# Kernel optimization log

Measured on AMD Instinct MI355X. Metric: run time of the kernel, lower is better.

The kernel has to match this reference:

```python
import jax, jax.numpy as jnp
import numpy as np

N_NODES = 65536
N_EDGES = 524288
N_LAYERS = 3
D = 128
ED = 32
BATCH = 64
NEG_SLOPE = 0.2


def setup_inputs() -> dict:
    key = jax.random.key(0)
    ks = jax.random.split(key, 10)
    w_scale = 1.0 / np.sqrt(D)
    return {
        "x": jax.random.normal(ks[0], (N_NODES, D), dtype=jnp.float32),
        "edge_index": jax.random.randint(ks[1], (2, N_EDGES), 0, N_NODES, dtype=jnp.int32),
        "edge_attr": jax.random.normal(ks[2], (N_EDGES, ED), dtype=jnp.float32),
        "Ws": jax.random.normal(ks[3], (N_LAYERS, D, D), dtype=jnp.float32) * w_scale,
        "att_src": jax.random.normal(ks[4], (N_LAYERS, D), dtype=jnp.float32) * w_scale,
        "att_dst": jax.random.normal(ks[5], (N_LAYERS, D), dtype=jnp.float32) * w_scale,
        "W_edge": jax.random.normal(ks[6], (N_LAYERS, ED, D), dtype=jnp.float32) * (1.0 / np.sqrt(ED)),
        "att_edge": jax.random.normal(ks[7], (N_LAYERS, D), dtype=jnp.float32) * w_scale,
        "bias": jnp.zeros((N_LAYERS, D), dtype=jnp.float32),
        "batch_size": BATCH,
    }


def _gat_layer(x, src, dst, ea, W, a_s, a_d, We, a_e, b, n):
    # PyG GATConv, heads=1, concat=True, flow source_to_target.
    h = x @ W                                      # [N, D]
    al = (h @ a_s)[src] + (h @ a_d)[dst] + (ea @ We) @ a_e   # [E]
    al = jax.nn.leaky_relu(al, NEG_SLOPE)
    # segment softmax over destination-node neighborhoods
    m = jax.ops.segment_max(al, dst, num_segments=n)
    ex = jnp.exp(al - m[dst])
    den = jax.ops.segment_sum(ex, dst, num_segments=n)
    w = ex / den[dst]                              # [E]
    out = jax.ops.segment_sum(w[:, None] * h[src], dst, num_segments=n)
    return out + b


def reference(x, edge_index, edge_attr, Ws, att_src, att_dst, W_edge, att_edge, bias, batch_size):
    n = x.shape[0]
    # add_self_loops with fill_value='mean': self-loop edge_attr is the mean of
    # incoming edge features per destination node (zero if no incoming edges).
    loop = jnp.arange(n, dtype=edge_index.dtype)
    src = jnp.concatenate([edge_index[0], loop])
    dst = jnp.concatenate([edge_index[1], loop])
    cnt = jax.ops.segment_sum(jnp.ones((edge_attr.shape[0],), edge_attr.dtype), edge_index[1], num_segments=n)
    fill = jax.ops.segment_sum(edge_attr, edge_index[1], num_segments=n) / jnp.maximum(cnt, 1.0)[:, None]
    ea = jnp.concatenate([edge_attr, fill], axis=0)

    h = x
    for l in range(Ws.shape[0]):
        h = jax.nn.gelu(
            _gat_layer(h, src, dst, ea, Ws[l], att_src[l], att_dst[l], W_edge[l], att_edge[l], bias[l], n),
            approximate=False,
        )
        # dropout p=0.2 is identity in eval mode
    return h.reshape(batch_size, n // batch_size, -1)
```

## Files before the change

### kernel.cpp

```cpp
#include <hip/hip_runtime.h>
#include <math.h>

#define NN 65536
#define NE 524288
#define D 128
#define ED 32
#define NEG_SLOPE 0.2f

typedef short bf16x8 __attribute__((ext_vector_type(8)));
typedef float f32x4 __attribute__((ext_vector_type(4)));
typedef unsigned short ushort_t;

__device__ __forceinline__ float leaky(float x) { return x > 0.f ? x : NEG_SLOPE * x; }
__device__ __forceinline__ float gelu_exact(float x) {
    return 0.5f * x * (1.f + erff(x * 0.70710678118654752440f));
}
__device__ __forceinline__ unsigned short bf16_rne(float x) {
    unsigned u = __float_as_uint(x);
    return (unsigned short)((u + 0x7FFFu + ((u >> 16) & 1u)) >> 16);
}
__device__ __forceinline__ void unpack8(int4 r, float* f) {
    unsigned u0 = (unsigned)r.x, u1 = (unsigned)r.y, u2 = (unsigned)r.z, u3 = (unsigned)r.w;
    f[0] = __uint_as_float(u0 << 16); f[1] = __uint_as_float(u0 & 0xFFFF0000u);
    f[2] = __uint_as_float(u1 << 16); f[3] = __uint_as_float(u1 & 0xFFFF0000u);
    f[4] = __uint_as_float(u2 << 16); f[5] = __uint_as_float(u2 & 0xFFFF0000u);
    f[6] = __uint_as_float(u3 << 16); f[7] = __uint_as_float(u3 & 0xFFFF0000u);
}


__global__ __launch_bounds__(256) void k_front(const float* __restrict__ ea,
        const int* __restrict__ srcArr,
        const float* __restrict__ We, const float* __restrict__ ae,
        const float* __restrict__ Ws, short* __restrict__ Whp, short* __restrict__ Wlp,
        int4* __restrict__ edata_eo) {
    if (blockIdx.x >= NE / 256) {
        int t = (blockIdx.x - NE / 256) * 256 + threadIdx.x;
        if (t >= 3 * 4 * 4 * 128) return;
        int n = t & 127;
        int q = (t >> 7) & 3;
        int ks = (t >> 9) & 3;
        int l = t >> 11;
        const float* w = Ws + (size_t)l * D * D;
        size_t obase = (size_t)l * D * D + ((size_t)((ks * 4 + q) * 128) + n) * 8;
        #pragma unroll
        for (int j = 0; j < 8; ++j) {
            float x = w[(size_t)(ks * 32 + q * 8 + j) * D + n];
            unsigned short hb = bf16_rne(x);
            float hf = __uint_as_float(((unsigned)hb) << 16);
            Whp[obase + j] = (short)hb;
            Wlp[obase + j] = (short)bf16_rne(x - hf);
        }
        return;
    }
    __shared__ __align__(16) float wv[3 * ED];
    int t = threadIdx.x;
    if (t < 3 * ED) {
        int l = t >> 5, k = t & 31;
        const float4* w = (const float4*)(We + (size_t)(l * ED + k) * D);
        const float4* a = (const float4*)(ae + (size_t)l * D);
        float s = 0.f;
        #pragma unroll
        for (int i = 0; i < D / 4; ++i) {
            float4 x = w[i], y = a[i];
            s += x.x * y.x + x.y * y.y + x.z * y.z + x.w * y.w;
        }
        wv[t] = s;
    }
    __syncthreads();

    int c = (t & 7) * 4;
    float4 wl0 = *(const float4*)(wv + c);
    float4 wl1 = *(const float4*)(wv + ED + c);
    float4 wl2 = *(const float4*)(wv + 2 * ED + c);
    const float4* eab = (const float4*)(ea + (size_t)blockIdx.x * 256 * ED);
    int rbase = blockIdx.x * 256;
    #pragma unroll
    for (int i = 0; i < 8; ++i) {
        float4 v = eab[i * 256 + t];
        float p0 = v.x * wl0.x + v.y * wl0.y + v.z * wl0.z + v.w * wl0.w;
        float p1 = v.x * wl1.x + v.y * wl1.y + v.z * wl1.z + v.w * wl1.w;
        float p2 = v.x * wl2.x + v.y * wl2.y + v.z * wl2.z + v.w * wl2.w;
        #pragma unroll
        for (int off = 1; off < 8; off <<= 1) {
            p0 += __shfl_xor(p0, off);
            p1 += __shfl_xor(p1, off);
            p2 += __shfl_xor(p2, off);
        }
        if ((t & 7) == 0) {
            int r = rbase + i * 32 + (t >> 3);
            edata_eo[r] = make_int4(srcArr[r], __float_as_int(p0),
                                    __float_as_int(p1), __float_as_int(p2));
        }
    }
}


__device__ __forceinline__ void gemm_body(int b, const float* __restrict__ A,
        const short* __restrict__ Whp, const short* __restrict__ Wlp,
        const float* __restrict__ a_s, const float* __restrict__ a_d,
        ushort_t* __restrict__ Hb, float* __restrict__ als, float* __restrict__ ald) {
    __shared__ int4 Bs[2048];
    int t = threadIdx.x;
    int wave = t >> 6, lane = t & 63;
    int l16 = lane & 15, q = lane >> 4;
    int rows_base = b * 64 + wave * 16;

    const int4* wh4 = (const int4*)Whp;
    const int4* wl4 = (const int4*)Wlp;
    const short* bsh = (const short*)Bs;
    const short* bsl = (const short*)(Bs + 1024);

    f32x4 acc[8] = {};
    #pragma unroll
    for (int h2 = 0; h2 < 2; ++h2) {
        if (h2) __syncthreads();
        #pragma unroll
        for (int i = 0; i < 4; ++i) {
            Bs[t + 256 * i] = wh4[h2 * 1024 + t + 256 * i];
            Bs[1024 + t + 256 * i] = wl4[h2 * 1024 + t + 256 * i];
        }
        __syncthreads();
        #pragma unroll
        for (int kk = 0; kk < 2; ++kk) {
            int ks = h2 * 2 + kk;
            const float* ap = A + (size_t)(rows_base + l16) * D + ks * 32 + q * 8;
            float4 v0 = *(const float4*)ap;
            float4 v1 = *(const float4*)(ap + 4);
            float f[8] = {v0.x, v0.y, v0.z, v0.w, v1.x, v1.y, v1.z, v1.w};
            bf16x8 ah, alo;
            #pragma unroll
            for (int j = 0; j < 8; ++j) {
                unsigned short hb = bf16_rne(f[j]);
                float hf = __uint_as_float(((unsigned)hb) << 16);
                ah[j]  = (short)hb;
                alo[j] = (short)bf16_rne(f[j] - hf);
            }
            #pragma unroll
            for (int nt = 0; nt < 8; ++nt) {
                int idx = (((kk * 4 + q) * 128) + nt * 16 + l16) * 8;
                bf16x8 bh = *(const bf16x8*)(bsh + idx);
                bf16x8 bl = *(const bf16x8*)(bsl + idx);
                acc[nt] = __builtin_amdgcn_mfma_f32_16x16x32_bf16(bh, ah, acc[nt], 0, 0, 0);
                acc[nt] = __builtin_amdgcn_mfma_f32_16x16x32_bf16(bl, ah, acc[nt], 0, 0, 0);
                acc[nt] = __builtin_amdgcn_mfma_f32_16x16x32_bf16(bh, alo, acc[nt], 0, 0, 0);
            }
        }
    }

    float ps = 0.f, pd = 0.f;
    #pragma unroll
    for (int nt = 0; nt < 8; ++nt) {
        float4 a4 = *(const float4*)(a_s + nt * 16 + q * 4);
        float4 d4 = *(const float4*)(a_d + nt * 16 + q * 4);
        ps += acc[nt][0] * a4.x + acc[nt][1] * a4.y + acc[nt][2] * a4.z + acc[nt][3] * a4.w;
        pd += acc[nt][0] * d4.x + acc[nt][1] * d4.y + acc[nt][2] * d4.z + acc[nt][3] * d4.w;
    }
    ps += __shfl_xor(ps, 16); pd += __shfl_xor(pd, 16);
    ps += __shfl_xor(ps, 32); pd += __shfl_xor(pd, 32);
    if (q == 0) {
        als[rows_base + l16] = ps;
        ald[rows_base + l16] = pd;
    }

    __syncthreads();
    char* tb = (char*)Bs + wave * 4096;
    {
        int row = l16;
        unsigned key = (unsigned)(row & 7) << 4;
        #pragma unroll
        for (int nt = 0; nt < 8; ++nt) {
            ushort4 pk;
            pk.x = bf16_rne(acc[nt][0]);
            pk.y = bf16_rne(acc[nt][1]);
            pk.z = bf16_rne(acc[nt][2]);
            pk.w = bf16_rne(acc[nt][3]);
            unsigned byteoff = (unsigned)row * 256u + (unsigned)(nt * 16 + q * 4) * 2u;
            *(ushort4*)(tb + (byteoff ^ key)) = pk;
        }
    }
    __syncthreads();
    #pragma unroll
    for (int i = 0; i < 4; ++i) {
        int m = lane + 64 * i;
        unsigned row = (unsigned)m >> 4;
        unsigned byteoff = (unsigned)m * 16u;
        unsigned addr = byteoff ^ ((row & 7u) << 4);
        int4 v = *(const int4*)(tb + addr);
        *(int4*)((char*)Hb + (size_t)rows_base * 256 + (size_t)m * 16) = v;
    }
}


__global__ __launch_bounds__(256) void k_h1g0(const int* __restrict__ dstArr,
        int* __restrict__ C,
        const float* __restrict__ x, const short* __restrict__ Whp,
        const short* __restrict__ Wlp, const float* __restrict__ a_s,
        const float* __restrict__ a_d, ushort_t* __restrict__ Hb,
        float* __restrict__ als, float* __restrict__ ald) {
    int t = threadIdx.x;
    if (blockIdx.x < 512) {
        __shared__ int hist[256];
        hist[t] = 0;
        __syncthreads();
        int base = blockIdx.x * 1024;
        #pragma unroll
        for (int i = 0; i < 4; ++i) {
            int d = dstArr[base + i * 256 + t];
            atomicAdd(&hist[d >> 8], 1);
        }
        __syncthreads();
        C[blockIdx.x * 256 + t] = hist[t];
        return;
    }
    gemm_body(blockIdx.x - 512, x, Whp, Wlp, a_s, a_d, Hb, als, ald);
}


__global__ __launch_bounds__(256) void k_scanA(int* __restrict__ C, int* __restrict__ T) {
    __shared__ int s[512];
    int t = threadIdx.x, h = blockIdx.x;
    int a0 = C[t * 256 + h];
    int a1 = C[(t + 256) * 256 + h];
    s[t] = a0; s[t + 256] = a1;
    __syncthreads();
    for (int off = 1; off < 512; off <<= 1) {
        int v0 = (t >= off) ? s[t - off] : 0;
        int v1 = (t + 256 >= off) ? s[t + 256 - off] : 0;
        __syncthreads();
        s[t] += v0; s[t + 256] += v1;
        __syncthreads();
    }
    C[t * 256 + h] = s[t] - a0;
    C[(t + 256) * 256 + h] = s[t + 256] - a1;
    if (t == 255) T[h] = s[511];
}


__global__ __launch_bounds__(256) void k_scanB(const int* __restrict__ T, int* __restrict__ H,
                                               int* __restrict__ rp) {
    __shared__ int s[256];
    int t = threadIdx.x;
    int v = T[t];
    s[t] = v;
    __syncthreads();
    for (int off = 1; off < 256; off <<= 1) {
        int x = (t >= off) ? s[t - off] : 0;
        __syncthreads();
        s[t] += x;
        __syncthreads();
    }
    H[t] = s[t] - v;
    if (t == 255) { H[256] = s[255]; rp[NN] = s[255]; }
}


__global__ __launch_bounds__(256) void k_rank1(const int* __restrict__ dstArr,
        const int4* __restrict__ edata_eo, const int* __restrict__ C,
        const int* __restrict__ H, int4* __restrict__ eordR, int* __restrict__ eordD) {
    __shared__ int base[256];
    __shared__ int cnt[256];
    int t = threadIdx.x, b = blockIdx.x;
    base[t] = C[b * 256 + t] + H[t];
    cnt[t] = 0;
    __syncthreads();
    #pragma unroll
    for (int i = 0; i < 4; ++i) {
        int e = b * 1024 + i * 256 + t;
        int d = dstArr[e];
        int4 rec = edata_eo[e];
        int hi = d >> 8;
        int r = atomicAdd(&cnt[hi], 1);
        int p = base[hi] + r;
        eordR[p] = rec;
        eordD[p] = d;
    }
}


__global__ __launch_bounds__(256) void k_rank2(const int* __restrict__ eordD,
        const int4* __restrict__ eordR, const int* __restrict__ H,
        int4* __restrict__ edata, int* __restrict__ rp) {
    __shared__ int h2[256];
    __shared__ int sc[256];
    __shared__ int cnt[256];
    int t = threadIdx.x, h = blockIdx.x;
    int s0 = H[h], s1 = H[h + 1];
    h2[t] = 0; cnt[t] = 0;
    __syncthreads();
    for (int i = s0 + t; i < s1; i += 256) atomicAdd(&h2[eordD[i] & 255], 1);
    __syncthreads();
    int v = h2[t];
    sc[t] = v;
    __syncthreads();
    for (int off = 1; off < 256; off <<= 1) {
        int x = (t >= off) ? sc[t - off] : 0;
        __syncthreads();
        sc[t] += x;
        __syncthreads();
    }
    int baseLo = sc[t] - v;
    rp[h * 256 + t] = s0 + baseLo;
    __syncthreads();
    sc[t] = baseLo;
    __syncthreads();
    for (int i = s0 + t; i < s1; i += 256) {
        int d = eordD[i];
        int4 rec = eordR[i];
        int lo = d & 255;
        int r = atomicAdd(&cnt[lo], 1);
        edata[s0 + sc[lo] + r] = rec;
    }
}


__global__ __launch_bounds__(256) void k_gemm(const float* __restrict__ A,
        const short* __restrict__ Whp, const short* __restrict__ Wlp,
        const float* __restrict__ a_s, const float* __restrict__ a_d,
        ushort_t* __restrict__ Hb, float* __restrict__ als, float* __restrict__ ald) {
    gemm_body(blockIdx.x, A, Whp, Wlp, a_s, a_d, Hb, als, ald);
}


__global__ __launch_bounds__(256) void k_aggr(const ushort_t* __restrict__ hb,
        const float* __restrict__ als, const float* __restrict__ ald,
        const int4* __restrict__ edata, const int* __restrict__ rp,
        const float* __restrict__ bias, int lsel, float* __restrict__ out_f32) {
    int t = threadIdx.x;
    int lane = t & 63;
    int l16 = lane & 15;
    int qb = lane & 48;
    int n = blockIdx.x * 16 + (t >> 4);
    int s = rp[n], e = rp[n + 1];
    int deg = e - s;
    float aldd = ald[n];
    float alsn = als[n];
    float inv_deg = (deg > 0) ? 1.f / (float)deg : 0.f;

    int4 hvp = *(const int4*)(hb + (size_t)n * D + l16 * 8);
    float acc8[8];

    if (deg <= 16) {
        int sn0 = 0;
        float alev0 = 0.f, alsg = 0.f;
        if (l16 < deg) {
            int4 ed = edata[s + l16];
            sn0 = ed.x;
            alev0 = __int_as_float((lsel == 0) ? ed.y : ((lsel == 1) ? ed.z : ed.w));
            alsg = als[sn0];
        }

        int sA[8], sB[8];
        #pragma unroll
        for (int i = 0; i < 8; ++i) { sA[i] = __shfl(sn0, qb + i); sB[i] = __shfl(sn0, qb + 8 + i); }
        int4 rb[8];
        #pragma unroll
        for (int i = 0; i < 8; ++i) rb[i] = *(const int4*)(hb + (size_t)sA[i] * D + l16 * 8);
        bool more = (deg > 8);
        int4 rb2[8];
        if (more) {
            #pragma unroll
            for (int i = 0; i < 8; ++i) rb2[i] = *(const int4*)(hb + (size_t)sB[i] * D + l16 * 8);
        }

        float al0 = (l16 < deg) ? leaky(alsg + aldd + alev0) : -1e30f;
        float mm = al0, asum = alev0;
        #pragma unroll
        for (int off = 1; off < 16; off <<= 1) {
            mm = fmaxf(mm, __shfl_xor(mm, off));
            asum += __shfl_xor(asum, off);
        }
        float self_al = leaky(alsn + aldd + asum * inv_deg);
        mm = fmaxf(mm, self_al);
        float p0 = (l16 < deg) ? __expf(al0 - mm) : 0.f;
        float den = p0;
        #pragma unroll
        for (int off = 1; off < 16; off <<= 1) den += __shfl_xor(den, off);
        float es = __expf(self_al - mm);
        den += es;
        float inv = 1.f / den;
        float w0 = p0 * inv;
        float wself = es * inv;

        float fv[8];
        unpack8(hvp, fv);
        #pragma unroll
        for (int j = 0; j < 8; ++j) acc8[j] = wself * fv[j];

        float wA[8], wB[8];
        #pragma unroll
        for (int i = 0; i < 8; ++i) { wA[i] = __shfl(w0, qb + i); wB[i] = __shfl(w0, qb + 8 + i); }

        #pragma unroll
        for (int i = 0; i < 8; ++i) {
            float f[8];
            unpack8(rb[i], f);
            #pragma unroll
            for (int j = 0; j < 8; ++j) acc8[j] += wA[i] * f[j];
        }
        if (more) {
            #pragma unroll
            for (int i = 0; i < 8; ++i) {
                float f[8];
                unpack8(rb2[i], f);
                #pragma unroll
                for (int j = 0; j < 8; ++j) acc8[j] += wB[i] * f[j];
            }
        }
    } else {
        float mm = -1e30f, asum = 0.f;
        for (int base = s; base < e; base += 16) {
            int j = base + l16;
            if (j < e) {
                int4 ed = edata[j];
                float alev = __int_as_float((lsel == 0) ? ed.y : ((lsel == 1) ? ed.z : ed.w));
                asum += alev;
                mm = fmaxf(mm, leaky(als[ed.x] + aldd + alev));
            }
        }
        #pragma unroll
        for (int off = 1; off < 16; off <<= 1) {
            mm = fmaxf(mm, __shfl_xor(mm, off));
            asum += __shfl_xor(asum, off);
        }
        float self_al = leaky(alsn + aldd + asum * inv_deg);
        mm = fmaxf(mm, self_al);
        float den = 0.f;
        for (int base = s; base < e; base += 16) {
            int j = base + l16;
            if (j < e) {
                int4 ed = edata[j];
                float alev = __int_as_float((lsel == 0) ? ed.y : ((lsel == 1) ? ed.z : ed.w));
                den += __expf(leaky(als[ed.x] + aldd + alev) - mm);
            }
        }
        #pragma unroll
        for (int off = 1; off < 16; off <<= 1) den += __shfl_xor(den, off);
        float es = __expf(self_al - mm);
        den += es;
        float inv = 1.f / den;
        float wself = es * inv;
        float fv[8];
        unpack8(hvp, fv);
        #pragma unroll
        for (int j = 0; j < 8; ++j) acc8[j] = wself * fv[j];
        for (int base = s; base < e; base += 16) {
            int cnt = min(e - base, 16);
            int sn = 0;
            float w = 0.f;
            if (l16 < cnt) {
                int4 ed = edata[base + l16];
                sn = ed.x;
                float alev = __int_as_float((lsel == 0) ? ed.y : ((lsel == 1) ? ed.z : ed.w));
                w = __expf(leaky(als[sn] + aldd + alev) - mm) * inv;
            }
            for (int tt = 0; tt < cnt; ++tt) {
                int st = __shfl(sn, qb + tt);
                float wt = __shfl(w, qb + tt);
                int4 r = *(const int4*)(hb + (size_t)st * D + l16 * 8);
                float f[8];
                unpack8(r, f);
                #pragma unroll
                for (int j = 0; j < 8; ++j) acc8[j] += wt * f[j];
            }
        }
    }

    const float4* b4 = (const float4*)(bias + l16 * 8);
    float4 b0 = b4[0], b1 = b4[1];
    float bb[8] = {b0.x, b0.y, b0.z, b0.w, b1.x, b1.y, b1.z, b1.w};
    float o[8];
    #pragma unroll
    for (int j = 0; j < 8; ++j) o[j] = gelu_exact(acc8[j] + bb[j]);

    float4* o4 = (float4*)(out_f32 + (size_t)n * D + l16 * 8);
    o4[0] = make_float4(o[0], o[1], o[2], o[3]);
    o4[1] = make_float4(o[4], o[5], o[6], o[7]);
}


extern "C" void kernel_launch(void* const* d_in, const int* in_sizes, int n_in,
                              void* d_out, int out_size, void* d_ws, size_t ws_size,
                              hipStream_t stream) {
    (void)in_sizes; (void)n_in; (void)out_size; (void)ws_size;
    const float* x        = (const float*)d_in[0];
    const int*   eidx     = (const int*)d_in[1];
    const float* ea       = (const float*)d_in[2];
    const float* Ws       = (const float*)d_in[3];
    const float* att_src  = (const float*)d_in[4];
    const float* att_dst  = (const float*)d_in[5];
    const float* W_edge   = (const float*)d_in[6];
    const float* att_edge = (const float*)d_in[7];
    const float* bias     = (const float*)d_in[8];
    float* out = (float*)d_out;

    char* ws = (char*)d_ws;
    size_t off = 0;
    auto alloc = [&](size_t bytes) {
        void* p = ws + off;
        off += (bytes + 255) & ~(size_t)255;
        return p;
    };
    ushort_t* Hb   = (ushort_t*)alloc((size_t)NN * D * 2);
    float*    Hx   = (float*)alloc((size_t)NN * D * 4);
    float*    als  = (float*)alloc((size_t)NN * 4);
    float*    ald  = (float*)alloc((size_t)NN * 4);
    int4*     edata= (int4*)alloc((size_t)(NE + 16) * 16);
    int4*     edata_eo = (int4*)alloc((size_t)NE * 16);
    int4*     eordR = (int4*)alloc((size_t)NE * 16);
    int*      eordD = (int*)alloc((size_t)NE * 4);
    int*      C    = (int*)alloc((size_t)512 * 256 * 4);
    int*      T    = (int*)alloc(256 * 4);
    int*      H    = (int*)alloc(260 * 4);
    int*      rp   = (int*)alloc((size_t)(NN + 4) * 4);
    short*    Whp  = (short*)alloc((size_t)3 * D * D * 2);
    short*    Wlp  = (short*)alloc((size_t)3 * D * D * 2);

    const int* e_src = eidx;
    const int* e_dst = eidx + NE;

    k_front<<<NE / 256 + 24, 256, 0, stream>>>(ea, e_src, W_edge, att_edge,
                                               Ws, Whp, Wlp, edata_eo);
    k_h1g0<<<512 + NN / 64, 256, 0, stream>>>(e_dst, C, x, Whp, Wlp, att_src, att_dst,
                                              Hb, als, ald);
    k_scanA<<<256, 256, 0, stream>>>(C, T);
    k_scanB<<<256 / 256, 256, 0, stream>>>(T, H, rp);
    k_rank1<<<512, 256, 0, stream>>>(e_dst, edata_eo, C, H, eordR, eordD);
    k_rank2<<<256, 256, 0, stream>>>(eordD, eordR, H, edata, rp);

    for (int l = 0; l < 3; ++l) {
        bool last = (l == 2);
        k_aggr<<<NN / 16, 256, 0, stream>>>(Hb, als, ald, edata, rp, bias + (size_t)l * D, l,
                                            last ? out : Hx);
        if (!last) {
            k_gemm<<<NN / 64, 256, 0, stream>>>(Hx, Whp + (size_t)(l + 1) * D * D,
                                                Wlp + (size_t)(l + 1) * D * D,
                                                att_src + (size_t)(l + 1) * D,
                                                att_dst + (size_t)(l + 1) * D,
                                                Hb, als, ald);
        }
    }
}
```

Before: 349.9 us.

## Fuse edge-attention projection into partition scatter and drop intermediate edge buffer

The edge-attribute projection onto the three per-layer edge attention vectors now happens inside the bucket-scatter kernel. Each block computes the projections and writes the packed records straight into their destination-bucketed slots, so the separate edge-record buffer no longer has to be written and read back. The destination histogram and weight packing move into a small first kernel that runs before the scans. The scatter is fused with the first-layer GEMM in a single launch so the two can overlap. In exchange, each scatter block walks 1024 edges serially with only one lane in eight doing atomics, and the order of edges within a bucket changes.

```diff
diff --git a/kernel.cpp b/kernel.cpp
--- a/kernel.cpp
+++ b/kernel.cpp
@@ -28,70 +28,78 @@
 }
 
 
-__global__ __launch_bounds__(256) void k_front(const float* __restrict__ ea,
-        const int* __restrict__ srcArr,
-        const float* __restrict__ We, const float* __restrict__ ae,
-        const float* __restrict__ Ws, short* __restrict__ Whp, short* __restrict__ Wlp,
-        int4* __restrict__ edata_eo) {
-    if (blockIdx.x >= NE / 256) {
-        int t = (blockIdx.x - NE / 256) * 256 + threadIdx.x;
-        if (t >= 3 * 4 * 4 * 128) return;
-        int n = t & 127;
-        int q = (t >> 7) & 3;
-        int ks = (t >> 9) & 3;
-        int l = t >> 11;
-        const float* w = Ws + (size_t)l * D * D;
-        size_t obase = (size_t)l * D * D + ((size_t)((ks * 4 + q) * 128) + n) * 8;
-        #pragma unroll
-        for (int j = 0; j < 8; ++j) {
-            float x = w[(size_t)(ks * 32 + q * 8 + j) * D + n];
-            unsigned short hb = bf16_rne(x);
-            float hf = __uint_as_float(((unsigned)hb) << 16);
-            Whp[obase + j] = (short)hb;
-            Wlp[obase + j] = (short)bf16_rne(x - hf);
-        }
+__global__ __launch_bounds__(256) void k_hist_wpack(const int* __restrict__ dstArr,
+        int* __restrict__ C, const float* __restrict__ Ws,
+        short* __restrict__ Whp, short* __restrict__ Wlp) {
+    int t = threadIdx.x;
+    if (blockIdx.x < 512) {
+        __shared__ int hist[256];
+        hist[t] = 0;
+        __syncthreads();
+        int base = blockIdx.x * 1024;
+        #pragma unroll
+        for (int i = 0; i < 4; ++i) {
+            int d = dstArr[base + i * 256 + t];
+            atomicAdd(&hist[d >> 8], 1);
+        }
+        __syncthreads();
+        C[blockIdx.x * 256 + t] = hist[t];
         return;
     }
-    __shared__ __align__(16) float wv[3 * ED];
+    int tt = (blockIdx.x - 512) * 256 + t;
+    if (tt >= 3 * 4 * 4 * 128) return;
+    int n = tt & 127;
+    int q = (tt >> 7) & 3;
+    int ks = (tt >> 9) & 3;
+    int l = tt >> 11;
+    const float* w = Ws + (size_t)l * D * D;
+    size_t obase = (size_t)l * D * D + ((size_t)((ks * 4 + q) * 128) + n) * 8;
+    #pragma unroll
+    for (int j = 0; j < 8; ++j) {
+        float x = w[(size_t)(ks * 32 + q * 8 + j) * D + n];
+        unsigned short hb = bf16_rne(x);
+        float hf = __uint_as_float(((unsigned)hb) << 16);
+        Whp[obase + j] = (short)hb;
+        Wlp[obase + j] = (short)bf16_rne(x - hf);
+    }
+}
+
+
+__global__ __launch_bounds__(256) void k_scanA(int* __restrict__ C, int* __restrict__ T) {
+    __shared__ int s[512];
+    int t = threadIdx.x, h = blockIdx.x;
+    int a0 = C[t * 256 + h];
+    int a1 = C[(t + 256) * 256 + h];
+    s[t] = a0; s[t + 256] = a1;
+    __syncthreads();
+    for (int off = 1; off < 512; off <<= 1) {
+        int v0 = (t >= off) ? s[t - off] : 0;
+        int v1 = (t + 256 >= off) ? s[t + 256 - off] : 0;
+        __syncthreads();
+        s[t] += v0; s[t + 256] += v1;
+        __syncthreads();
+    }
+    C[t * 256 + h] = s[t] - a0;
+    C[(t + 256) * 256 + h] = s[t + 256] - a1;
+    if (t == 255) T[h] = s[511];
+}
+
+
+__global__ __launch_bounds__(256) void k_scanB(const int* __restrict__ T, int* __restrict__ H,
+                                               int* __restrict__ rp) {
+    __shared__ int s[256];
     int t = threadIdx.x;
-    if (t < 3 * ED) {
-        int l = t >> 5, k = t & 31;
-        const float4* w = (const float4*)(We + (size_t)(l * ED + k) * D);
-        const float4* a = (const float4*)(ae + (size_t)l * D);
-        float s = 0.f;
-        #pragma unroll
-        for (int i = 0; i < D / 4; ++i) {
-            float4 x = w[i], y = a[i];
-            s += x.x * y.x + x.y * y.y + x.z * y.z + x.w * y.w;
-        }
-        wv[t] = s;
-    }
-    __syncthreads();
-
-    int c = (t & 7) * 4;
-    float4 wl0 = *(const float4*)(wv + c);
-    float4 wl1 = *(const float4*)(wv + ED + c);
-    float4 wl2 = *(const float4*)(wv + 2 * ED + c);
-    const float4* eab = (const float4*)(ea + (size_t)blockIdx.x * 256 * ED);
-    int rbase = blockIdx.x * 256;
-    #pragma unroll
-    for (int i = 0; i < 8; ++i) {
-        float4 v = eab[i * 256 + t];
-        float p0 = v.x * wl0.x + v.y * wl0.y + v.z * wl0.z + v.w * wl0.w;
-        float p1 = v.x * wl1.x + v.y * wl1.y + v.z * wl1.z + v.w * wl1.w;
-        float p2 = v.x * wl2.x + v.y * wl2.y + v.z * wl2.z + v.w * wl2.w;
-        #pragma unroll
-        for (int off = 1; off < 8; off <<= 1) {
-            p0 += __shfl_xor(p0, off);
-            p1 += __shfl_xor(p1, off);
-            p2 += __shfl_xor(p2, off);
-        }
-        if ((t & 7) == 0) {
-            int r = rbase + i * 32 + (t >> 3);
-            edata_eo[r] = make_int4(srcArr[r], __float_as_int(p0),
-                                    __float_as_int(p1), __float_as_int(p2));
-        }
-    }
+    int v = T[t];
+    s[t] = v;
+    __syncthreads();
+    for (int off = 1; off < 256; off <<= 1) {
+        int x = (t >= off) ? s[t - off] : 0;
+        __syncthreads();
+        s[t] += x;
+        __syncthreads();
+    }
+    H[t] = s[t] - v;
+    if (t == 255) { H[256] = s[255]; rp[NN] = s[255]; }
 }
 
 
@@ -191,89 +199,68 @@
 }
 
 
-__global__ __launch_bounds__(256) void k_h1g0(const int* __restrict__ dstArr,
-        int* __restrict__ C,
+__global__ __launch_bounds__(256) void k_partgemm(const float* __restrict__ ea,
+        const int* __restrict__ srcArr, const int* __restrict__ dstArr,
+        const float* __restrict__ We, const float* __restrict__ ae,
+        const int* __restrict__ C, const int* __restrict__ H,
+        int4* __restrict__ eordR, int* __restrict__ eordD,
         const float* __restrict__ x, const short* __restrict__ Whp,
         const short* __restrict__ Wlp, const float* __restrict__ a_s,
         const float* __restrict__ a_d, ushort_t* __restrict__ Hb,
         float* __restrict__ als, float* __restrict__ ald) {
     int t = threadIdx.x;
     if (blockIdx.x < 512) {
-        __shared__ int hist[256];
-        hist[t] = 0;
-        __syncthreads();
-        int base = blockIdx.x * 1024;
-        #pragma unroll
-        for (int i = 0; i < 4; ++i) {
-            int d = dstArr[base + i * 256 + t];
-            atomicAdd(&hist[d >> 8], 1);
-        }
-        __syncthreads();
-        C[blockIdx.x * 256 + t] = hist[t];
+        __shared__ __align__(16) float wv[3 * ED];
+        __shared__ int sbase[256];
+        __shared__ int scnt[256];
+        if (t < 3 * ED) {
+            int l = t >> 5, k = t & 31;
+            const float4* w = (const float4*)(We + (size_t)(l * ED + k) * D);
+            const float4* a = (const float4*)(ae + (size_t)l * D);
+            float s = 0.f;
+            #pragma unroll
+            for (int i = 0; i < D / 4; ++i) {
+                float4 xx = w[i], yy = a[i];
+                s += xx.x * yy.x + xx.y * yy.y + xx.z * yy.z + xx.w * yy.w;
+            }
+            wv[t] = s;
+        }
+        sbase[t] = C[blockIdx.x * 256 + t] + H[t];
+        scnt[t] = 0;
+        __syncthreads();
+
+        int c = (t & 7) * 4;
+        float4 wl0 = *(const float4*)(wv + c);
+        float4 wl1 = *(const float4*)(wv + ED + c);
+        float4 wl2 = *(const float4*)(wv + 2 * ED + c);
+        const float4* eab = (const float4*)(ea + (size_t)blockIdx.x * 1024 * ED);
+        int rbase = blockIdx.x * 1024;
+        #pragma unroll 4
+        for (int i = 0; i < 32; ++i) {
+            float4 v = eab[i * 256 + t];
+            float p0 = v.x * wl0.x + v.y * wl0.y + v.z * wl0.z + v.w * wl0.w;
+            float p1 = v.x * wl1.x + v.y * wl1.y + v.z * wl1.z + v.w * wl1.w;
+            float p2 = v.x * wl2.x + v.y * wl2.y + v.z * wl2.z + v.w * wl2.w;
+            #pragma unroll
+            for (int off = 1; off < 8; off <<= 1) {
+                p0 += __shfl_xor(p0, off);
+                p1 += __shfl_xor(p1, off);
+                p2 += __shfl_xor(p2, off);
+            }
+            if ((t & 7) == 0) {
+                int r = rbase + i * 32 + (t >> 3);
+                int d = dstArr[r];
+                int hi = d >> 8;
+                int rk = atomicAdd(&scnt[hi], 1);
+                int p = sbase[hi] + rk;
+                eordR[p] = make_int4(srcArr[r], __float_as_int(p0),
+                                     __float_as_int(p1), __float_as_int(p2));
+                eordD[p] = d;
+            }
+        }
         return;
     }
     gemm_body(blockIdx.x - 512, x, Whp, Wlp, a_s, a_d, Hb, als, ald);
-}
-
-
-__global__ __launch_bounds__(256) void k_scanA(int* __restrict__ C, int* __restrict__ T) {
-    __shared__ int s[512];
-    int t = threadIdx.x, h = blockIdx.x;
-    int a0 = C[t * 256 + h];
-    int a1 = C[(t + 256) * 256 + h];
-    s[t] = a0; s[t + 256] = a1;
-    __syncthreads();
-    for (int off = 1; off < 512; off <<= 1) {
-        int v0 = (t >= off) ? s[t - off] : 0;
-        int v1 = (t + 256 >= off) ? s[t + 256 - off] : 0;
-        __syncthreads();
-        s[t] += v0; s[t + 256] += v1;
-        __syncthreads();
-    }
-    C[t * 256 + h] = s[t] - a0;
-    C[(t + 256) * 256 + h] = s[t + 256] - a1;
-    if (t == 255) T[h] = s[511];
-}
-
-
-__global__ __launch_bounds__(256) void k_scanB(const int* __restrict__ T, int* __restrict__ H,
-                                               int* __restrict__ rp) {
-    __shared__ int s[256];
-    int t = threadIdx.x;
-    int v = T[t];
-    s[t] = v;
-    __syncthreads();
-    for (int off = 1; off < 256; off <<= 1) {
-        int x = (t >= off) ? s[t - off] : 0;
-        __syncthreads();
-        s[t] += x;
-        __syncthreads();
-    }
-    H[t] = s[t] - v;
-    if (t == 255) { H[256] = s[255]; rp[NN] = s[255]; }
-}
-
-
-__global__ __launch_bounds__(256) void k_rank1(const int* __restrict__ dstArr,
-        const int4* __restrict__ edata_eo, const int* __restrict__ C,
-        const int* __restrict__ H, int4* __restrict__ eordR, int* __restrict__ eordD) {
-    __shared__ int base[256];
-    __shared__ int cnt[256];
-    int t = threadIdx.x, b = blockIdx.x;
-    base[t] = C[b * 256 + t] + H[t];
-    cnt[t] = 0;
-    __syncthreads();
-    #pragma unroll
-    for (int i = 0; i < 4; ++i) {
-        int e = b * 1024 + i * 256 + t;
-        int d = dstArr[e];
-        int4 rec = edata_eo[e];
-        int hi = d >> 8;
-        int r = atomicAdd(&cnt[hi], 1);
-        int p = base[hi] + r;
-        eordR[p] = rec;
-        eordD[p] = d;
-    }
 }
 
 
@@ -505,7 +492,6 @@
     float*    als  = (float*)alloc((size_t)NN * 4);
     float*    ald  = (float*)alloc((size_t)NN * 4);
     int4*     edata= (int4*)alloc((size_t)(NE + 16) * 16);
-    int4*     edata_eo = (int4*)alloc((size_t)NE * 16);
     int4*     eordR = (int4*)alloc((size_t)NE * 16);
     int*      eordD = (int*)alloc((size_t)NE * 4);
     int*      C    = (int*)alloc((size_t)512 * 256 * 4);
@@ -518,13 +504,13 @@
     const int* e_src = eidx;
     const int* e_dst = eidx + NE;
 
-    k_front<<<NE / 256 + 24, 256, 0, stream>>>(ea, e_src, W_edge, att_edge,
-                                               Ws, Whp, Wlp, edata_eo);
-    k_h1g0<<<512 + NN / 64, 256, 0, stream>>>(e_dst, C, x, Whp, Wlp, att_src, att_dst,
-                                              Hb, als, ald);
+    k_hist_wpack<<<512 + 24, 256, 0, stream>>>(e_dst, C, Ws, Whp, Wlp);
     k_scanA<<<256, 256, 0, stream>>>(C, T);
-    k_scanB<<<256 / 256, 256, 0, stream>>>(T, H, rp);
-    k_rank1<<<512, 256, 0, stream>>>(e_dst, edata_eo, C, H, eordR, eordD);
+    k_scanB<<<1, 256, 0, stream>>>(T, H, rp);
+    k_partgemm<<<512 + NN / 64, 256, 0, stream>>>(ea, e_src, e_dst, W_edge, att_edge,
+                                                  C, H, eordR, eordD,
+                                                  x, Whp, Wlp, att_src, att_dst,
+                                                  Hb, als, ald);
     k_rank2<<<256, 256, 0, stream>>>(eordD, eordR, H, edata, rp);
 
     for (int l = 0; l < 3; ++l) {
```

Result: slower. 381.6 us (+9.1%).
